# Kernel tuning notes

Hardware: AMD Instinct MI355X
Metric: run time of the kernel (lower is better)

Reference implementation:

```python
import jax, jax.numpy as jnp
import numpy as np

WS = 7            # window size
DISP = WS // 2    # cyclic shift displacement = 3
N_HEAD = 6
DIM_V = 32
DIM_MODEL = 192

def _gen_mask(ws, d, upper_lower=False, left_right=False):
    w2 = ws * ws
    m = np.zeros((w2, w2), np.float32)
    if upper_lower:
        m[-d * ws:, :-d * ws] = -np.inf
        m[:-d * ws, -d * ws:] = -np.inf
    if left_right:
        m = m.reshape(ws, ws, ws, ws)
        m[:, -d:, :, :-d] = -np.inf
        m[:, :-d, :, -d:] = -np.inf
        m = m.reshape(w2, w2)
    return jnp.asarray(m)

def _rel_indices(ws):
    idx = np.array([[a, b] for a in range(ws) for b in range(ws)])
    rel = idx[None, :, :] - idx[:, None, :] + ws - 1   # (ws^2, ws^2, 2)
    return jnp.asarray(rel[:, :, 0]), jnp.asarray(rel[:, :, 1])

LOWER_MASK = _gen_mask(WS, DISP, upper_lower=True)
RIGHT_MASK = _gen_mask(WS, DISP, left_right=True)
REL_I, REL_J = _rel_indices(WS)

def setup_inputs() -> dict:
    key = jax.random.key(0)
    ks = jax.random.split(key, 6)
    x = jax.random.normal(ks[0], (32, 56, 56, DIM_MODEL), jnp.float32)
    Wq = jax.random.normal(ks[1], (DIM_MODEL, DIM_V * N_HEAD), jnp.float32) * 0.02
    Wk = jax.random.normal(ks[2], (DIM_MODEL, DIM_V * N_HEAD), jnp.float32) * 0.02
    Wv = jax.random.normal(ks[3], (DIM_MODEL, DIM_V * N_HEAD), jnp.float32) * 0.02
    Wfc = jax.random.normal(ks[4], (DIM_V * N_HEAD, DIM_MODEL), jnp.float32) * 0.02
    bfc = jnp.zeros((DIM_MODEL,), jnp.float32)
    pos_embedding = jax.random.normal(ks[5], (2 * WS - 1, 2 * WS - 1), jnp.float32)
    return {"x": x, "Wq": Wq, "Wk": Wk, "Wv": Wv, "Wfc": Wfc, "bfc": bfc,
            "pos_embedding": pos_embedding}

def reference(x, Wq, Wk, Wv, Wfc, bfc, pos_embedding):
    # cyclic shift (shifted=True)
    x = jnp.roll(x, (-DISP, -DISP), (1, 2))
    b, n_h, n_w, _ = x.shape
    wh, ww = n_h // WS, n_w // WS          # 8, 8
    nw = wh * ww                            # 64 windows
    q = x @ Wq
    k = x @ Wk
    v = x @ Wv
    # faithful raw .view (NOT spatial window partition)
    shp = (b, N_HEAD, nw, WS * WS, DIM_V)
    q = q.reshape(shp)
    k = k.reshape(shp)
    v = v.reshape(shp)
    # note: original MULTIPLIES by sqrt(dim_v)
    scores = jnp.einsum('bhnqd,bhnkd->bhnqk', q, k) * (DIM_V ** 0.5)
    # relative position bias gather: (ws^2, ws^2)
    bias = pos_embedding[REL_I, REL_J]
    scores = scores + bias
    # shifted-window masks on specific window indices
    scores = scores.at[:, :, -ww:].add(LOWER_MASK)
    scores = scores.at[:, :, ww - 1:ww].add(RIGHT_MASK)
    attn = jax.nn.softmax(scores, axis=-1)
    out = jnp.einsum('bhnqk,bhnkd->bhnqd', attn, v)
    out = out.reshape(b, n_h, n_w, -1)
    out = out @ Wfc + bfc
    out = jnp.roll(out, (DISP, DISP), (1, 2))
    return out
```

## Files before the change

kernel.cpp:

```cpp
#include <hip/hip_runtime.h>
#include <hip/hip_bf16.h>

typedef __attribute__((ext_vector_type(8))) short bf16x8;
typedef __attribute__((ext_vector_type(4))) short bf16x4;
typedef __attribute__((ext_vector_type(4))) float f32x4;


__device__ __forceinline__ short f2bf(float f) {
  __bf16 h = (__bf16)f;
  unsigned short u;
  __builtin_memcpy(&u, &h, 2);
  return (short)u;
}
__device__ __forceinline__ int swz(int f) { return f ^ (((f >> 6) & 7) << 3); }

__global__ void prep_kernel(const float* __restrict__ Wq, const float* __restrict__ Wk,
                            const float* __restrict__ Wv, const float* __restrict__ Wfc,
                            const float* __restrict__ pos,
                            short* __restrict__ WTf, short* __restrict__ WfcTf,
                            float* __restrict__ biasP) {
  int i0 = blockIdx.x * blockDim.x + threadIdx.x;
  int stride = gridDim.x * blockDim.x;
  for (int o = i0; o < 110592; o += stride) {
    int e = o & 7, ln = (o >> 3) & 63, t = o >> 9;
    int ks = t % 6, ct = t / 6;
    int col = ct * 16 + (ln & 15);
    int k = ks * 32 + ((ln >> 4) << 3) + e;
    const float* W = (col < 192) ? Wq : (col < 384) ? Wk : Wv;
    WTf[o] = f2bf(W[k * 192 + (col % 192)]);
  }
  for (int o = i0; o < 36864; o += stride) {
    int e = o & 7, ln = (o >> 3) & 63, t = o >> 9;
    int ks = t % 6, ct = t / 6;
    int col = ct * 16 + (ln & 15);
    int k = ks * 32 + ((ln >> 4) << 3) + e;
    WfcTf[o] = f2bf(Wfc[k * 192 + col]);
  }
  for (int idx = i0; idx < 12288; idx += stride) {
    int jj = idx & 3, ln = (idx >> 2) & 63, kt = (idx >> 8) & 3;
    int qt = (idx >> 10) & 3, t = idx >> 12;
    int kk = kt * 16 + ((ln >> 4) << 2) + jj;
    int qq = qt * 16 + (ln & 15);
    float v;
    if (kk >= 49 || qq >= 49) {
      v = -1e30f;
    } else {
      int ri = kk / 7 - qq / 7 + 6;
      int rj = kk % 7 - qq % 7 + 6;
      v = pos[ri * 13 + rj] * 1.4426950408889634f;
      if (t == 1 && ((qq >= 28) != (kk >= 28))) v = -1e30f;
      if (t == 2 && ((qq % 7 >= 4) != (kk % 7 >= 4))) v = -1e30f;
    }
    biasP[idx] = v;
  }
}

__launch_bounds__(1024, 1)
__global__ void swin_fused(const float* __restrict__ x,
                           const short* __restrict__ WTf,
                           const short* __restrict__ WfcTf,
                           const float* __restrict__ biasP,
                           const float* __restrict__ bfc,
                           float* __restrict__ out) {
  __shared__ short qf[18816];
  __shared__ short kf[18816];
  __shared__ short vT[24576];

  const int bid = blockIdx.x;
  const int tid = threadIdx.x;
  const int wave = tid >> 6;
  const int lane = tid & 63;
  const int sub = (wave >= 8) ? 1 : 0;
  const int wl = wave - sub * 8;
  const int gg = bid * 2 + sub;
  const int b = gg >> 6;
  const int gl = gg & 63;
  const int lrow = lane & 15;
  const int lk8 = (lane >> 4) << 3;
  const int lg4 = (lane >> 4) << 2;
  const int qoff = sub * 9408;
  const int voff = sub * 12288;

  const bf16x8 z8 = {0, 0, 0, 0, 0, 0, 0, 0};
  const f32x4 z4 = {0.f, 0.f, 0.f, 0.f};

  for (int i = tid; i < 2 * 2880; i += 1024) {
    int s = (i >= 2880) ? 1 : 0;
    int r = i - s * 2880;
    int wd = r / 15, tok = 49 + (r - wd * 15);
    vT[s * 12288 + swz(wd * 64 + tok)] = 0;
  }

  const int mh2 = wl & 1;
  const int cw = wl >> 1;
  {
    bf16x8 afrag[2][6];
    #pragma unroll
    for (int mh = 0; mh < 2; ++mh) {
      int row = mh2 * 32 + mh * 16 + lrow;
      if (row < 49) {
        int t = gl * 49 + row;
        int h = t / 56, w = t - h * 56;
        int hs = h + 3; if (hs >= 56) hs -= 56;
        int ws2 = w + 3; if (ws2 >= 56) ws2 -= 56;
        const float* xr = x + ((b * 56 + hs) * 56 + ws2) * 192 + lk8;
        #pragma unroll
        for (int ks = 0; ks < 6; ++ks) {
          float4 f0 = *(const float4*)(xr + 32 * ks);
          float4 f1 = *(const float4*)(xr + 32 * ks + 4);
          bf16x8 a;
          a[0] = f2bf(f0.x); a[1] = f2bf(f0.y); a[2] = f2bf(f0.z); a[3] = f2bf(f0.w);
          a[4] = f2bf(f1.x); a[5] = f2bf(f1.y); a[6] = f2bf(f1.z); a[7] = f2bf(f1.w);
          afrag[mh][ks] = a;
        }
      } else {
        #pragma unroll
        for (int ks = 0; ks < 6; ++ks) afrag[mh][ks] = z8;
      }
    }

    auto p1_load = [&](bf16x8 (&bfr)[6], int ct) {
      const short* wr = WTf + ct * 3072 + (lane << 3);
      #pragma unroll
      for (int ks = 0; ks < 6; ++ks) bfr[ks] = *(const bf16x8*)(wr + ks * 512);
    };
    auto p1_tile = [&](const bf16x8 (&bfr)[6], int ct) {
      f32x4 acc0 = z4, acc1 = z4;
      __builtin_amdgcn_s_setprio(1);
      #pragma unroll
      for (int ks = 0; ks < 6; ++ks) {
        acc0 = __builtin_amdgcn_mfma_f32_16x16x32_bf16(bfr[ks], afrag[0][ks], acc0, 0, 0, 0);
        acc1 = __builtin_amdgcn_mfma_f32_16x16x32_bf16(bfr[ks], afrag[1][ks], acc1, 0, 0, 0);
      }
      __builtin_amdgcn_s_setprio(0);
      if (ct < 12) {
        int cbase = ct * 16 + lg4;
        #pragma unroll
        for (int mh = 0; mh < 2; ++mh) {
          f32x4 a4 = mh ? acc1 : acc0;
          int tok = mh2 * 32 + mh * 16 + lrow;
          if (tok < 49) {
            bf16x4 v = {f2bf(a4[0] * 8.16111560867f), f2bf(a4[1] * 8.16111560867f),
                        f2bf(a4[2] * 8.16111560867f), f2bf(a4[3] * 8.16111560867f)};
            *(bf16x4*)(qf + qoff + swz(tok * 192 + cbase)) = v;
          }
        }
      } else if (ct < 24) {
        int cbase = (ct - 12) * 16 + lg4;
        #pragma unroll
        for (int mh = 0; mh < 2; ++mh) {
          f32x4 a4 = mh ? acc1 : acc0;
          int tok = mh2 * 32 + mh * 16 + lrow;
          if (tok < 49) {
            bf16x4 v = {f2bf(a4[0]), f2bf(a4[1]), f2bf(a4[2]), f2bf(a4[3])};
            *(bf16x4*)(kf + qoff + swz(tok * 192 + cbase)) = v;
          }
        }
      } else {
        int cbase = (ct - 24) * 16 + lg4;
        #pragma unroll
        for (int mh = 0; mh < 2; ++mh) {
          f32x4 a4 = mh ? acc1 : acc0;
          int tok = mh2 * 32 + mh * 16 + lrow;
          if (tok < 49) {
            int flat0 = tok * 192 + cbase;
            int w2 = flat0 / 1568;
            int rem0 = flat0 - w2 * 1568;
            int base0 = (w2 * 32 + (rem0 & 31)) * 64 + (rem0 >> 5);
            vT[voff + swz(base0)]       = f2bf(a4[0]);
            vT[voff + swz(base0 + 64)]  = f2bf(a4[1]);
            vT[voff + swz(base0 + 128)] = f2bf(a4[2]);
            vT[voff + swz(base0 + 192)] = f2bf(a4[3]);
          }
        }
      }
    };

    bf16x8 bA[6], bB[6];
    p1_load(bA, cw);
    #pragma unroll 1
    for (int nt = 0; nt < 8; nt += 2) {
      p1_load(bB, (nt + 1) * 4 + cw);
      p1_tile(bA, nt * 4 + cw);
      if (nt + 2 < 9) p1_load(bA, (nt + 2) * 4 + cw);
      p1_tile(bB, (nt + 1) * 4 + cw);
    }
    p1_tile(bA, 32 + cw);
  }
  __syncthreads();

  #pragma unroll 1
  for (int u3 = 0; u3 < 3; ++u3) {
    int u = wl * 3 + u3;
    int win = u >> 2, qt = u & 3;
    int qbase = win * 1568;
    int gwin = (gl * 6 + win) & 63;
    int tsel = (gwin >= 56) ? 1 : (gwin == 7) ? 2 : 0;

    const float* bp = biasP + ((tsel * 4 + qt) * 4) * 256 + (lane << 2);
    f32x4 bv[4];
    #pragma unroll
    for (int kt = 0; kt < 4; ++kt)
      bv[kt] = *(const f32x4*)(bp + kt * 256);

    bf16x8 ka[4];
    #pragma unroll
    for (int kt = 0; kt < 4; ++kt) {
      int row = kt * 16 + lrow;
      ka[kt] = (row < 49) ? *(const bf16x8*)(kf + qoff + swz(qbase + row * 32 + lk8)) : z8;
    }

    int qq = qt * 16 + lrow;
    bf16x8 qb = (qq < 49) ? *(const bf16x8*)(qf + qoff + swz(qbase + qq * 32 + lk8)) : z8;
    f32x4 st[4];
    __builtin_amdgcn_s_setprio(1);
    #pragma unroll
    for (int kt = 0; kt < 4; ++kt)
      st[kt] = __builtin_amdgcn_mfma_f32_16x16x32_bf16(ka[kt], qb, z4, 0, 0, 0);
    __builtin_amdgcn_s_setprio(0);

    float s4[4];
    #pragma unroll
    for (int kt = 0; kt < 4; ++kt) {
      #pragma unroll
      for (int jj = 0; jj < 4; ++jj) {
        float e = exp2f(st[kt][jj] + bv[kt][jj]);
        st[kt][jj] = e;
      }
      s4[kt] = (st[kt][0] + st[kt][1]) + (st[kt][2] + st[kt][3]);
    }
    float sum = (s4[0] + s4[1]) + (s4[2] + s4[3]);
    sum += __shfl_xor(sum, 16);
    sum += __shfl_xor(sum, 32);
    float inv = 1.0f / sum;

    bf16x4 pb[4];
    #pragma unroll
    for (int kt = 0; kt < 4; ++kt) {
      bf16x4 p = {f2bf(st[kt][0]), f2bf(st[kt][1]), f2bf(st[kt][2]), f2bf(st[kt][3])};
      pb[kt] = p;
    }

    bf16x4 va[2][4];
    #pragma unroll
    for (int dt = 0; dt < 2; ++dt)
      #pragma unroll
      for (int kt = 0; kt < 4; ++kt)
        va[dt][kt] = *(const bf16x4*)(vT + voff + swz((win * 32 + dt * 16 + lrow) * 64 + kt * 16 + lg4));

    #pragma unroll
    for (int dt = 0; dt < 2; ++dt) {
      f32x4 oo = z4;
#if __has_builtin(__builtin_amdgcn_mfma_f32_16x16x16bf16_1k)
      #pragma unroll
      for (int kt = 0; kt < 4; ++kt)
        oo = __builtin_amdgcn_mfma_f32_16x16x16bf16_1k(va[dt][kt], pb[kt], oo, 0, 0, 0);
#else
      #pragma unroll
      for (int kt = 0; kt < 4; ++kt) {
        bf16x8 va8 = {va[dt][kt][0], va[dt][kt][1], va[dt][kt][2], va[dt][kt][3], 0, 0, 0, 0};
        bf16x8 pb8 = {pb[kt][0], pb[kt][1], pb[kt][2], pb[kt][3], 0, 0, 0, 0};
        oo = __builtin_amdgcn_mfma_f32_16x16x32_bf16(va8, pb8, oo, 0, 0, 0);
      }
#endif
      if (qq < 49) {
        bf16x4 ov = {f2bf(oo[0] * inv), f2bf(oo[1] * inv), f2bf(oo[2] * inv), f2bf(oo[3] * inv)};
        *(bf16x4*)(qf + qoff + swz(qbase + qq * 32 + dt * 16 + lg4)) = ov;
      }
    }
  }
  __syncthreads();

  {
    const int wq = wl >> 1;
    f32x4 acc[2][3];
    #pragma unroll
    for (int mi = 0; mi < 2; ++mi)
      #pragma unroll
      for (int nc = 0; nc < 3; ++nc) acc[mi][nc] = z4;

    auto p3_load = [&](bf16x8 (&wf)[3], int ks) {
      #pragma unroll
      for (int nc = 0; nc < 3; ++nc)
        wf[nc] = *(const bf16x8*)(WfcTf + ((wq * 3 + nc) * 6 + ks) * 512 + (lane << 3));
    };
    auto p3_step = [&](const bf16x8 (&wf)[3], int ks) {
      bf16x8 oa[2];
      #pragma unroll
      for (int mi = 0; mi < 2; ++mi) {
        int row = mh2 * 32 + mi * 16 + lrow;
        oa[mi] = (row < 49) ? *(const bf16x8*)(qf + qoff + swz(row * 192 + ks * 32 + lk8)) : z8;
      }
      __builtin_amdgcn_s_setprio(1);
      #pragma unroll
      for (int nc = 0; nc < 3; ++nc)
        #pragma unroll
        for (int mi = 0; mi < 2; ++mi)
          acc[mi][nc] = __builtin_amdgcn_mfma_f32_16x16x32_bf16(wf[nc], oa[mi], acc[mi][nc], 0, 0, 0);
      __builtin_amdgcn_s_setprio(0);
    };

    bf16x8 wA[3], wB[3];
    p3_load(wA, 0);
    #pragma unroll 1
    for (int ks = 0; ks < 6; ks += 2) {
      p3_load(wB, ks + 1);
      p3_step(wA, ks);
      if (ks + 2 < 6) p3_load(wA, ks + 2);
      p3_step(wB, ks + 1);
    }

    const int colb = wq * 48 + lg4;
    f32x4 bias[3];
    #pragma unroll
    for (int nc = 0; nc < 3; ++nc)
      bias[nc] = *(const f32x4*)(bfc + colb + nc * 16);
    #pragma unroll
    for (int mi = 0; mi < 2; ++mi) {
      int tok = mh2 * 32 + mi * 16 + lrow;
      if (tok < 49) {
        int t = gl * 49 + tok;
        int h = t / 56, w = t - h * 56;
        int hd = h + 3; if (hd >= 56) hd -= 56;
        int wd = w + 3; if (wd >= 56) wd -= 56;
        float* orow = out + (size_t)((b * 56 + hd) * 56 + wd) * 192 + colb;
        #pragma unroll
        for (int nc = 0; nc < 3; ++nc) {
          f32x4 v = acc[mi][nc] + bias[nc];
          *(f32x4*)(orow + nc * 16) = v;
        }
      }
    }
  }
}

extern "C" void kernel_launch(void* const* d_in, const int* in_sizes, int n_in,
                              void* d_out, int out_size, void* d_ws, size_t ws_size,
                              hipStream_t stream) {
  const float* x   = (const float*)d_in[0];
  const float* Wq  = (const float*)d_in[1];
  const float* Wk  = (const float*)d_in[2];
  const float* Wv  = (const float*)d_in[3];
  const float* Wfc = (const float*)d_in[4];
  const float* bfc = (const float*)d_in[5];
  const float* pos = (const float*)d_in[6];

  short* WTf   = (short*)d_ws;
  short* WfcTf = (short*)((char*)d_ws + 221184);
  float* biasP = (float*)((char*)d_ws + 294912);

  hipLaunchKernelGGL(prep_kernel, dim3(128), dim3(256), 0, stream,
                     Wq, Wk, Wv, Wfc, pos, WTf, WfcTf, biasP);
  hipLaunchKernelGGL(swin_fused, dim3(1024), dim3(1024), 0, stream,
                     x, WTf, WfcTf, biasP, bfc, (float*)d_out);
}
```

Baseline: 121.6 us.

## Split fused Swin kernel into QKV projection and attention kernels via workspace

Replaces the single fused 1024-thread kernel with two kernels. The first projects Q, K and V and writes them to global workspace in bf16. The second computes windowed attention and the output projection. Each block now handles one 49-token group with 512 threads and much less LDS, which aims to raise occupancy and drop the long single-kernel critical path. In exchange it adds roughly 127 MB of global-memory round trips and a second launch, and it only runs when the workspace is large enough.

```diff
diff --git a/kernel.cpp b/kernel.cpp
--- a/kernel.cpp
+++ b/kernel.cpp
@@ -5,6 +5,10 @@
 typedef __attribute__((ext_vector_type(4))) short bf16x4;
 typedef __attribute__((ext_vector_type(4))) float f32x4;
 
+#define QG_OFF   344064u
+#define KG_OFF   (QG_OFF + 38535168u)
+#define VB_OFF   (KG_OFF + 38535168u)
+#define WS_NEEDED ((size_t)VB_OFF + 50331648u)
 
 __device__ __forceinline__ short f2bf(float f) {
   __bf16 h = (__bf16)f;
@@ -55,6 +59,301 @@
   }
 }
 
+__launch_bounds__(512)
+__global__ void qkv_kernel(const float* __restrict__ x,
+                           const short* __restrict__ WTf,
+                           short* __restrict__ qg, short* __restrict__ kg,
+                           short* __restrict__ vb) {
+  const int gg = blockIdx.x;
+  const int b = gg >> 6;
+  const int gl = gg & 63;
+  const int tid = threadIdx.x;
+  const int wl = tid >> 6;
+  const int lane = tid & 63;
+  const int lrow = lane & 15;
+  const int lk8 = (lane >> 4) << 3;
+  const int lg4 = (lane >> 4) << 2;
+  const int mh2 = wl & 1;
+  const int cw = wl >> 1;
+
+  short* qgp = qg + gg * 9408;
+  short* kgp = kg + gg * 9408;
+  short* vbp = vb + gg * 12288;
+
+  const bf16x8 z8 = {0, 0, 0, 0, 0, 0, 0, 0};
+  const f32x4 z4 = {0.f, 0.f, 0.f, 0.f};
+
+  for (int i = tid; i < 2880; i += 512) {
+    int wd = i / 15, tok = 49 + (i - wd * 15);
+    vbp[wd * 64 + tok] = 0;
+  }
+
+  bf16x8 afrag[2][6];
+  #pragma unroll
+  for (int mh = 0; mh < 2; ++mh) {
+    int row = mh2 * 32 + mh * 16 + lrow;
+    if (row < 49) {
+      int t = gl * 49 + row;
+      int h = t / 56, w = t - h * 56;
+      int hs = h + 3; if (hs >= 56) hs -= 56;
+      int ws2 = w + 3; if (ws2 >= 56) ws2 -= 56;
+      const float* xr = x + ((b * 56 + hs) * 56 + ws2) * 192 + lk8;
+      #pragma unroll
+      for (int ks = 0; ks < 6; ++ks) {
+        float4 f0 = *(const float4*)(xr + 32 * ks);
+        float4 f1 = *(const float4*)(xr + 32 * ks + 4);
+        bf16x8 a;
+        a[0] = f2bf(f0.x); a[1] = f2bf(f0.y); a[2] = f2bf(f0.z); a[3] = f2bf(f0.w);
+        a[4] = f2bf(f1.x); a[5] = f2bf(f1.y); a[6] = f2bf(f1.z); a[7] = f2bf(f1.w);
+        afrag[mh][ks] = a;
+      }
+    } else {
+      #pragma unroll
+      for (int ks = 0; ks < 6; ++ks) afrag[mh][ks] = z8;
+    }
+  }
+
+  auto p1_load = [&](bf16x8 (&bfr)[6], int ct) {
+    const short* wr = WTf + ct * 3072 + (lane << 3);
+    #pragma unroll
+    for (int ks = 0; ks < 6; ++ks) bfr[ks] = *(const bf16x8*)(wr + ks * 512);
+  };
+  auto p1_tile = [&](const bf16x8 (&bfr)[6], int ct) {
+    f32x4 acc0 = z4, acc1 = z4;
+    __builtin_amdgcn_s_setprio(1);
+    #pragma unroll
+    for (int ks = 0; ks < 6; ++ks) {
+      acc0 = __builtin_amdgcn_mfma_f32_16x16x32_bf16(bfr[ks], afrag[0][ks], acc0, 0, 0, 0);
+      acc1 = __builtin_amdgcn_mfma_f32_16x16x32_bf16(bfr[ks], afrag[1][ks], acc1, 0, 0, 0);
+    }
+    __builtin_amdgcn_s_setprio(0);
+    if (ct < 12) {
+      int cbase = ct * 16 + lg4;
+      #pragma unroll
+      for (int mh = 0; mh < 2; ++mh) {
+        f32x4 a4 = mh ? acc1 : acc0;
+        int tok = mh2 * 32 + mh * 16 + lrow;
+        if (tok < 49) {
+          bf16x4 v = {f2bf(a4[0] * 8.16111560867f), f2bf(a4[1] * 8.16111560867f),
+                      f2bf(a4[2] * 8.16111560867f), f2bf(a4[3] * 8.16111560867f)};
+          *(bf16x4*)(qgp + tok * 192 + cbase) = v;
+        }
+      }
+    } else if (ct < 24) {
+      int cbase = (ct - 12) * 16 + lg4;
+      #pragma unroll
+      for (int mh = 0; mh < 2; ++mh) {
+        f32x4 a4 = mh ? acc1 : acc0;
+        int tok = mh2 * 32 + mh * 16 + lrow;
+        if (tok < 49) {
+          bf16x4 v = {f2bf(a4[0]), f2bf(a4[1]), f2bf(a4[2]), f2bf(a4[3])};
+          *(bf16x4*)(kgp + tok * 192 + cbase) = v;
+        }
+      }
+    } else {
+      int cbase = (ct - 24) * 16 + lg4;
+      #pragma unroll
+      for (int mh = 0; mh < 2; ++mh) {
+        f32x4 a4 = mh ? acc1 : acc0;
+        int tok = mh2 * 32 + mh * 16 + lrow;
+        if (tok < 49) {
+          int flat0 = tok * 192 + cbase;
+          int w2 = flat0 / 1568;
+          int rem0 = flat0 - w2 * 1568;
+          int base0 = (w2 * 32 + (rem0 & 31)) * 64 + (rem0 >> 5);
+          vbp[base0]       = f2bf(a4[0]);
+          vbp[base0 + 64]  = f2bf(a4[1]);
+          vbp[base0 + 128] = f2bf(a4[2]);
+          vbp[base0 + 192] = f2bf(a4[3]);
+        }
+      }
+    }
+  };
+
+  bf16x8 bA[6], bB[6];
+  p1_load(bA, cw);
+  #pragma unroll 1
+  for (int nt = 0; nt < 8; nt += 2) {
+    p1_load(bB, (nt + 1) * 4 + cw);
+    p1_tile(bA, nt * 4 + cw);
+    if (nt + 2 < 9) p1_load(bA, (nt + 2) * 4 + cw);
+    p1_tile(bB, (nt + 1) * 4 + cw);
+  }
+  p1_tile(bA, 32 + cw);
+}
+
+__launch_bounds__(512)
+__global__ void attn_kernel(const short* __restrict__ qg, const short* __restrict__ kg,
+                            const short* __restrict__ vb,
+                            const float* __restrict__ biasP,
+                            const short* __restrict__ WfcTf,
+                            const float* __restrict__ bfc,
+                            float* __restrict__ out) {
+  __shared__ short ao[9408];
+
+  const int gg = blockIdx.x;
+  const int b = gg >> 6;
+  const int gl = gg & 63;
+  const int tid = threadIdx.x;
+  const int wl = tid >> 6;
+  const int lane = tid & 63;
+  const int lrow = lane & 15;
+  const int lk8 = (lane >> 4) << 3;
+  const int lg4 = (lane >> 4) << 2;
+  const int mh2 = wl & 1;
+
+  const short* qgp = qg + gg * 9408;
+  const short* kgp = kg + gg * 9408;
+  const short* vbp = vb + gg * 12288;
+
+  const bf16x8 z8 = {0, 0, 0, 0, 0, 0, 0, 0};
+  const f32x4 z4 = {0.f, 0.f, 0.f, 0.f};
+
+  #pragma unroll 1
+  for (int u3 = 0; u3 < 3; ++u3) {
+    int u = wl * 3 + u3;
+    int win = u >> 2, qt = u & 3;
+    int qbase = win * 1568;
+    int gwin = (gl * 6 + win) & 63;
+    int tsel = (gwin >= 56) ? 1 : (gwin == 7) ? 2 : 0;
+
+    const float* bp = biasP + ((tsel * 4 + qt) * 4) * 256 + (lane << 2);
+    f32x4 bv[4];
+    #pragma unroll
+    for (int kt = 0; kt < 4; ++kt)
+      bv[kt] = *(const f32x4*)(bp + kt * 256);
+
+    bf16x8 ka[4];
+    #pragma unroll
+    for (int kt = 0; kt < 4; ++kt) {
+      int row = kt * 16 + lrow;
+      ka[kt] = (row < 49) ? *(const bf16x8*)(kgp + qbase + row * 32 + lk8) : z8;
+    }
+
+    int qq = qt * 16 + lrow;
+    bf16x8 qb = (qq < 49) ? *(const bf16x8*)(qgp + qbase + qq * 32 + lk8) : z8;
+    f32x4 st[4];
+    __builtin_amdgcn_s_setprio(1);
+    #pragma unroll
+    for (int kt = 0; kt < 4; ++kt)
+      st[kt] = __builtin_amdgcn_mfma_f32_16x16x32_bf16(ka[kt], qb, z4, 0, 0, 0);
+    __builtin_amdgcn_s_setprio(0);
+
+    float s4[4];
+    #pragma unroll
+    for (int kt = 0; kt < 4; ++kt) {
+      #pragma unroll
+      for (int jj = 0; jj < 4; ++jj) {
+        float e = exp2f(st[kt][jj] + bv[kt][jj]);
+        st[kt][jj] = e;
+      }
+      s4[kt] = (st[kt][0] + st[kt][1]) + (st[kt][2] + st[kt][3]);
+    }
+    float sum = (s4[0] + s4[1]) + (s4[2] + s4[3]);
+    sum += __shfl_xor(sum, 16);
+    sum += __shfl_xor(sum, 32);
+    float inv = 1.0f / sum;
+
+    bf16x4 pb[4];
+    #pragma unroll
+    for (int kt = 0; kt < 4; ++kt) {
+      bf16x4 p = {f2bf(st[kt][0]), f2bf(st[kt][1]), f2bf(st[kt][2]), f2bf(st[kt][3])};
+      pb[kt] = p;
+    }
+
+    bf16x4 va[2][4];
+    #pragma unroll
+    for (int dt = 0; dt < 2; ++dt)
+      #pragma unroll
+      for (int kt = 0; kt < 4; ++kt)
+        va[dt][kt] = *(const bf16x4*)(vbp + (win * 32 + dt * 16 + lrow) * 64 + kt * 16 + lg4);
+
+    #pragma unroll
+    for (int dt = 0; dt < 2; ++dt) {
+      f32x4 oo = z4;
+#if __has_builtin(__builtin_amdgcn_mfma_f32_16x16x16bf16_1k)
+      #pragma unroll
+      for (int kt = 0; kt < 4; ++kt)
+        oo = __builtin_amdgcn_mfma_f32_16x16x16bf16_1k(va[dt][kt], pb[kt], oo, 0, 0, 0);
+#else
+      #pragma unroll
+      for (int kt = 0; kt < 4; ++kt) {
+        bf16x8 va8 = {va[dt][kt][0], va[dt][kt][1], va[dt][kt][2], va[dt][kt][3], 0, 0, 0, 0};
+        bf16x8 pb8 = {pb[kt][0], pb[kt][1], pb[kt][2], pb[kt][3], 0, 0, 0, 0};
+        oo = __builtin_amdgcn_mfma_f32_16x16x32_bf16(va8, pb8, oo, 0, 0, 0);
+      }
+#endif
+      if (qq < 49) {
+        bf16x4 ov = {f2bf(oo[0] * inv), f2bf(oo[1] * inv), f2bf(oo[2] * inv), f2bf(oo[3] * inv)};
+        *(bf16x4*)(ao + swz(qbase + qq * 32 + dt * 16 + lg4)) = ov;
+      }
+    }
+  }
+  __syncthreads();
+
+  {
+    const int wq = wl >> 1;
+    f32x4 acc[2][3];
+    #pragma unroll
+    for (int mi = 0; mi < 2; ++mi)
+      #pragma unroll
+      for (int nc = 0; nc < 3; ++nc) acc[mi][nc] = z4;
+
+    auto p3_load = [&](bf16x8 (&wf)[3], int ks) {
+      #pragma unroll
+      for (int nc = 0; nc < 3; ++nc)
+        wf[nc] = *(const bf16x8*)(WfcTf + ((wq * 3 + nc) * 6 + ks) * 512 + (lane << 3));
+    };
+    auto p3_step = [&](const bf16x8 (&wf)[3], int ks) {
+      bf16x8 oa[2];
+      #pragma unroll
+      for (int mi = 0; mi < 2; ++mi) {
+        int row = mh2 * 32 + mi * 16 + lrow;
+        oa[mi] = (row < 49) ? *(const bf16x8*)(ao + swz(row * 192 + ks * 32 + lk8)) : z8;
+      }
+      __builtin_amdgcn_s_setprio(1);
+      #pragma unroll
+      for (int nc = 0; nc < 3; ++nc)
+        #pragma unroll
+        for (int mi = 0; mi < 2; ++mi)
+          acc[mi][nc] = __builtin_amdgcn_mfma_f32_16x16x32_bf16(wf[nc], oa[mi], acc[mi][nc], 0, 0, 0);
+      __builtin_amdgcn_s_setprio(0);
+    };
+
+    bf16x8 wA[3], wB[3];
+    p3_load(wA, 0);
+    #pragma unroll 1
+    for (int ks = 0; ks < 6; ks += 2) {
+      p3_load(wB, ks + 1);
+      p3_step(wA, ks);
+      if (ks + 2 < 6) p3_load(wA, ks + 2);
+      p3_step(wB, ks + 1);
+    }
+
+    const int colb = wq * 48 + lg4;
+    f32x4 bias[3];
+    #pragma unroll
+    for (int nc = 0; nc < 3; ++nc)
+      bias[nc] = *(const f32x4*)(bfc + colb + nc * 16);
+    #pragma unroll
+    for (int mi = 0; mi < 2; ++mi) {
+      int tok = mh2 * 32 + mi * 16 + lrow;
+      if (tok < 49) {
+        int t = gl * 49 + tok;
+        int h = t / 56, w = t - h * 56;
+        int hd = h + 3; if (hd >= 56) hd -= 56;
+        int wd = w + 3; if (wd >= 56) wd -= 56;
+        float* orow = out + (size_t)((b * 56 + hd) * 56 + wd) * 192 + colb;
+        #pragma unroll
+        for (int nc = 0; nc < 3; ++nc) {
+          f32x4 v = acc[mi][nc] + bias[nc];
+          *(f32x4*)(orow + nc * 16) = v;
+        }
+      }
+    }
+  }
+}
+
 __launch_bounds__(1024, 1)
 __global__ void swin_fused(const float* __restrict__ x,
                            const short* __restrict__ WTf,
@@ -351,6 +650,17 @@
 
   hipLaunchKernelGGL(prep_kernel, dim3(128), dim3(256), 0, stream,
                      Wq, Wk, Wv, Wfc, pos, WTf, WfcTf, biasP);
-  hipLaunchKernelGGL(swin_fused, dim3(1024), dim3(1024), 0, stream,
-                     x, WTf, WfcTf, biasP, bfc, (float*)d_out);
+
+  if (ws_size >= WS_NEEDED) {
+    short* qg = (short*)((char*)d_ws + QG_OFF);
+    short* kg = (short*)((char*)d_ws + KG_OFF);
+    short* vb = (short*)((char*)d_ws + VB_OFF);
+    hipLaunchKernelGGL(qkv_kernel, dim3(2048), dim3(512), 0, stream,
+                       x, WTf, qg, kg, vb);
+    hipLaunchKernelGGL(attn_kernel, dim3(2048), dim3(512), 0, stream,
+                       qg, kg, vb, biasP, WfcTf, bfc, (float*)d_out);
+  } else {
+    hipLaunchKernelGGL(swin_fused, dim3(1024), dim3(1024), 0, stream,
+                       x, WTf, WfcTf, biasP, bfc, (float*)d_out);
+  }
 }
```

Result: slower. 206.8 us (+70.1%).
